# Kernel tuning notes

Hardware: AMD Instinct MI355X
Metric: run time of the kernel (lower is better)

The kernel has to match this reference:

```python
import jax, jax.numpy as jnp
import numpy as np

DIM = 768
NUM_HEADS = 12
HEAD_DIM = DIM // NUM_HEADS
SCALE = HEAD_DIM ** -0.5
KEEP_NUM = 160


def setup_inputs() -> dict:
    key = jax.random.key(0)
    k0, k1, k2, k3 = jax.random.split(key, 4)
    B, N, C = 64, 197, DIM
    x = jax.random.normal(k0, (B, N, C), dtype=jnp.float32)
    # torch nn.Linear weights: [out_features, in_features]
    qkv_w = jax.random.normal(k1, (3 * C, C), dtype=jnp.float32) * (C ** -0.5)
    proj_w = jax.random.normal(k2, (C, C), dtype=jnp.float32) * (C ** -0.5)
    proj_b = jax.random.normal(k3, (C,), dtype=jnp.float32) * 0.01
    return {"x": x, "qkv_w": qkv_w, "proj_w": proj_w, "proj_b": proj_b}


def reference(x, qkv_w, proj_w, proj_b):
    B, N, C = x.shape
    H, D = NUM_HEADS, HEAD_DIM
    # qkv: [B, N, 3, H, D] -> q,k,v each [B, H, N, D]
    qkv = (x @ qkv_w.T).reshape(B, N, 3, H, D)
    qkv = jnp.transpose(qkv, (2, 0, 3, 1, 4))
    q, k, v = qkv[0], qkv[1], qkv[2]
    # raw pre-softmax scores [B, H, N, N]
    attn = jnp.einsum('bhnd,bhmd->bhnm', q, k) * SCALE
    # SUM_ABS_1: CLS row of scores, abs-summed over heads -> [B, N]
    attn_weight = jnp.sum(jnp.abs(attn[:, :, 0, :]), axis=1)
    # top_pool: keep top KEEP_NUM tokens by weight, indices sorted ascending
    _, idx = jax.lax.top_k(attn_weight, KEEP_NUM)
    keep_index = jnp.sort(idx, axis=-1)
    # standard attention
    attn = jax.nn.softmax(attn, axis=-1)
    out = jnp.einsum('bhnm,bhmd->bhnd', attn, v)
    out = jnp.transpose(out, (0, 2, 1, 3)).reshape(B, N, C)
    out = out @ proj_w.T + proj_b
    return out, keep_index
```

## Files before the change

### kernel.cpp

```cpp
#include <hip/hip_runtime.h>
#include <hip/hip_bf16.h>


#define BB 64
#define NN 197
#define CC 768
#define HH 12
#define DD 64
#define KEEP 160
#define SCALE_F 0.125f
#define OUT0_ELEMS ((size_t)BB * NN * CC)
#define VST 212

typedef __attribute__((ext_vector_type(8))) short bf16x8_t;
typedef __attribute__((ext_vector_type(4))) float f32x4_t;

__device__ __forceinline__ float b2f(unsigned short u) {
  union { unsigned u; float f; } cv; cv.u = (unsigned)u << 16; return cv.f;
}
__device__ __forceinline__ unsigned short f2b(float f) {
  union { float f; unsigned u; } cv; cv.f = f;
  return (unsigned short)((cv.u + 0x7FFFu + ((cv.u >> 16) & 1u)) >> 16);
}
__device__ __forceinline__ float ldmix(const void* p, size_t i, int f32) {
  return f32 ? ((const float*)p)[i] : b2f(((const unsigned short*)p)[i]);
}
__device__ __forceinline__ bf16x8_t ld8(const unsigned short* p) {
  short4 a = *(const short4*)p;
  short4 b = *(const short4*)(p + 4);
  bf16x8_t v = {a.x, a.y, a.z, a.w, b.x, b.y, b.z, b.w};
  return v;
}
__device__ __forceinline__ void gload16(const unsigned short* g,
                                        unsigned short* s) {
  __builtin_amdgcn_global_load_lds(
      (const __attribute__((address_space(1))) void*)g,
      (__attribute__((address_space(3))) void*)s, 16, 0, 0);
}

__global__ void detect_kernel(const void* x, int* flag) {
  __shared__ int cnt;
  if (threadIdx.x == 0) cnt = 0;
  __syncthreads();
  const unsigned short* u = (const unsigned short*)x;
  int wild = 0;
  for (int i = threadIdx.x; i < 4096; i += 256) {
    int e = (u[i] >> 7) & 0xFF;
    wild += (e >= 140);
  }
  atomicAdd(&cnt, wild);
  __syncthreads();
  if (threadIdx.x == 0) *flag = (cnt > 100) ? 1 : 0;
}

__global__ void cvt_all(const void* qkv_w, const void* proj_w, const void* proj_b,
                        unsigned short* wb, unsigned short* pw, float* pbf,
                        const int* flag) {
  const int W3 = 3 * CC * CC, W1 = CC * CC;
  int i = blockIdx.x * 256 + threadIdx.x;
  const int f32 = *flag;
  if (i < W3) {
    wb[i] = f32 ? f2b(((const float*)qkv_w)[i]) : ((const unsigned short*)qkv_w)[i];
  } else if (i < W3 + W1) {
    int j = i - W3;
    pw[j] = f32 ? f2b(((const float*)proj_w)[j]) : ((const unsigned short*)proj_w)[j];
  } else if (i < W3 + W1 + CC) {
    int j = i - W3 - W1;
    pbf[j] = ldmix(proj_b, j, f32);
  }
}

__global__ void cvt_x(const void* __restrict__ x, size_t elem_off,
                      unsigned short* __restrict__ xb, int n8,
                      const int* __restrict__ flag) {
  const int i = blockIdx.x * 256 + threadIdx.x;
  if (i >= n8) return;
  const size_t src = elem_off + (size_t)i * 8;
  bf16x8_t v;
  if (*flag) {
    const float* xp = (const float*)x + src;
    float4 u0 = *(const float4*)xp;
    float4 u1 = *(const float4*)(xp + 4);
    v = bf16x8_t{(short)f2b(u0.x), (short)f2b(u0.y), (short)f2b(u0.z),
                 (short)f2b(u0.w), (short)f2b(u1.x), (short)f2b(u1.y),
                 (short)f2b(u1.z), (short)f2b(u1.w)};
  } else {
    v = *(const bf16x8_t*)((const unsigned short*)x + src);
  }
  *(bf16x8_t*)(xb + (size_t)i * 8) = v;
}

__global__ __launch_bounds__(256, 4) void qkv_gemm(
    const unsigned short* __restrict__ xb,
    const unsigned short* __restrict__ wb,
    unsigned short* __restrict__ qkvc, int Mc, int bc, int nRow) {
  const int xcd = blockIdx.x & 7;
  const int seq = blockIdx.x >> 3;
  const int colt = seq % 18;
  const int rowt = (seq / 18) * 8 + xcd;
  if (rowt >= nRow) return;
  const int m0 = rowt * 128;
  const int n0 = colt * 128;

  __shared__ unsigned short As[4096];
  __shared__ unsigned short Bs[4096];
  const int lane = threadIdx.x & 63;
  const int wave = threadIdx.x >> 6;
  const int l16  = lane & 15;
  const int quad = lane >> 4;
  const int wm = wave >> 1, wn = wave & 1;

  const int rS   = wave * 16 + (lane >> 2);
  const int koff = (lane & 3) * 8;
  int grA0 = m0 + rS;       if (grA0 >= Mc) grA0 = Mc - 1;
  int grA1 = m0 + rS + 64;  if (grA1 >= Mc) grA1 = Mc - 1;
  const unsigned short* gA0 = xb + (size_t)grA0 * CC + koff;
  const unsigned short* gA1 = xb + (size_t)grA1 * CC + koff;
  const unsigned short* gB0 = wb + (size_t)(n0 + rS) * CC + koff;
  const unsigned short* gB1 = wb + (size_t)(n0 + rS + 64) * CC + koff;
  unsigned short* sA0 = As + wave * 512;
  unsigned short* sA1 = As + 2048 + wave * 512;
  unsigned short* sB0 = Bs + wave * 512;
  unsigned short* sB1 = Bs + 2048 + wave * 512;

  f32x4_t acc[4][4] = {};
  for (int kt = 0; kt < 24; kt++) {
    __syncthreads();
    gload16(gA0, sA0); gload16(gA1, sA1);
    gload16(gB0, sB0); gload16(gB1, sB1);
    gA0 += 32; gA1 += 32; gB0 += 32; gB1 += 32;
    __syncthreads();
    bf16x8_t afr[4], bfr[4];
    #pragma unroll
    for (int r = 0; r < 4; r++)
      afr[r] = *(const bf16x8_t*)&As[(wm * 4 + r) * 512 + l16 * 32 + quad * 8];
    #pragma unroll
    for (int c = 0; c < 4; c++)
      bfr[c] = *(const bf16x8_t*)&Bs[(wn * 4 + c) * 512 + l16 * 32 + quad * 8];
    #pragma unroll
    for (int r = 0; r < 4; r++)
      #pragma unroll
      for (int c = 0; c < 4; c++)
        acc[r][c] = __builtin_amdgcn_mfma_f32_16x16x32_bf16(afr[r], bfr[c],
                                                            acc[r][c], 0, 0, 0);
  }
  #pragma unroll
  for (int c = 0; c < 4; c++) {
    const int col = n0 + wn * 64 + c * 16 + l16;
    const int s = col / CC;
    const int rem = col - s * CC;
    const int hc = rem >> 6, d = rem & 63;
    #pragma unroll
    for (int r = 0; r < 4; r++) {
      #pragma unroll
      for (int i = 0; i < 4; i++) {
        const int m = m0 + wm * 64 + r * 16 + quad * 4 + i;
        if (m < Mc) {
          const int bb = m / NN, n = m - bb * NN;
          qkvc[((((size_t)s * bc + bb) * HH + hc) * NN + n) * DD + d] =
              f2b(acc[r][c][i]);
        }
      }
    }
  }
}

__global__ __launch_bounds__(256, 4) void proj_gemm(
    const unsigned short* __restrict__ Yc,
    const unsigned short* __restrict__ pw,
    const float* __restrict__ pbf,
    void* __restrict__ out, size_t out_off, int Mc, int nRow,
    const int* __restrict__ flag) {
  const int xcd = blockIdx.x & 7;
  const int seq = blockIdx.x >> 3;
  const int colt = seq % 6;
  const int rowt = (seq / 6) * 8 + xcd;
  if (rowt >= nRow) return;
  const int m0 = rowt * 128;
  const int n0 = colt * 128;

  __shared__ unsigned short As[4096];
  __shared__ unsigned short Bs[4096];
  const int lane = threadIdx.x & 63;
  const int wave = threadIdx.x >> 6;
  const int l16  = lane & 15;
  const int quad = lane >> 4;
  const int wm = wave >> 1, wn = wave & 1;

  const int rS   = wave * 16 + (lane >> 2);
  const int koff = (lane & 3) * 8;
  int grA0 = m0 + rS;       if (grA0 >= Mc) grA0 = Mc - 1;
  int grA1 = m0 + rS + 64;  if (grA1 >= Mc) grA1 = Mc - 1;
  const unsigned short* gA0 = Yc + (size_t)grA0 * CC + koff;
  const unsigned short* gA1 = Yc + (size_t)grA1 * CC + koff;
  const unsigned short* gB0 = pw + (size_t)(n0 + rS) * CC + koff;
  const unsigned short* gB1 = pw + (size_t)(n0 + rS + 64) * CC + koff;
  unsigned short* sA0 = As + wave * 512;
  unsigned short* sA1 = As + 2048 + wave * 512;
  unsigned short* sB0 = Bs + wave * 512;
  unsigned short* sB1 = Bs + 2048 + wave * 512;

  f32x4_t acc[4][4] = {};
  for (int kt = 0; kt < 24; kt++) {
    __syncthreads();
    gload16(gA0, sA0); gload16(gA1, sA1);
    gload16(gB0, sB0); gload16(gB1, sB1);
    gA0 += 32; gA1 += 32; gB0 += 32; gB1 += 32;
    __syncthreads();
    bf16x8_t afr[4], bfr[4];
    #pragma unroll
    for (int r = 0; r < 4; r++)
      afr[r] = *(const bf16x8_t*)&As[(wm * 4 + r) * 512 + l16 * 32 + quad * 8];
    #pragma unroll
    for (int c = 0; c < 4; c++)
      bfr[c] = *(const bf16x8_t*)&Bs[(wn * 4 + c) * 512 + l16 * 32 + quad * 8];
    #pragma unroll
    for (int r = 0; r < 4; r++)
      #pragma unroll
      for (int c = 0; c < 4; c++)
        acc[r][c] = __builtin_amdgcn_mfma_f32_16x16x32_bf16(afr[r], bfr[c],
                                                            acc[r][c], 0, 0, 0);
  }
  const int f32 = *flag;
  #pragma unroll
  for (int c = 0; c < 4; c++) {
    const int col = n0 + wn * 64 + c * 16 + l16;
    const float bv = pbf[col];
    #pragma unroll
    for (int r = 0; r < 4; r++) {
      #pragma unroll
      for (int i = 0; i < 4; i++) {
        const int m = m0 + wm * 64 + r * 16 + quad * 4 + i;
        if (m < Mc) {
          const float val = acc[r][c][i] + bv;
          const size_t oi = out_off + (size_t)m * CC + col;
          if (f32) ((float*)out)[oi] = val;
          else ((unsigned short*)out)[oi] = f2b(val);
        }
      }
    }
  }
}

__global__ __launch_bounds__(256, 3) void attn_kernel(
    const unsigned short* __restrict__ qkvc, int bc,
    unsigned short* __restrict__ Yc) {
  const int bh = blockIdx.x;
  const int bb = bh / HH;
  const int h  = bh % HH;
  const size_t mat = (size_t)bc * HH * NN * DD;
  const unsigned short* q = qkvc + ((size_t)bb * HH + h) * NN * DD;
  const unsigned short* k = q + mat;
  const unsigned short* v = q + 2 * mat;

  __shared__ unsigned short Vt[DD * VST];
  __shared__ unsigned short Pl[4][16 * VST];

  const int lane = threadIdx.x & 63;
  const int wave = threadIdx.x >> 6;
  const int l16  = lane & 15;
  const int quad = lane >> 4;

  #pragma unroll
  for (int it = 0; it < 53; it++) {
    const int key = it * 4 + wave;
    unsigned short val = (key < NN) ? v[(size_t)key * DD + lane]
                                    : (unsigned short)0;
    Vt[lane * VST + key] = val;
  }
  __syncthreads();

  unsigned short* Pw = &Pl[wave][0];

  for (int it = 0; it < 4; it++) {
    const int si = it * 4 + wave;
    if (si >= 13) break;
    const int q0 = si * 16;

    int qrow = q0 + l16; if (qrow >= NN) qrow = NN - 1;
    const unsigned short* qp = q + (size_t)qrow * DD + quad * 8;
    const bf16x8_t aq0 = *(const bf16x8_t*)qp;
    const bf16x8_t aq1 = *(const bf16x8_t*)(qp + 32);

    f32x4_t sc[13];
    #pragma unroll
    for (int ct = 0; ct < 13; ct++) {
      int key = ct * 16 + l16; if (key >= NN) key = NN - 1;
      const unsigned short* kp = k + (size_t)key * DD + quad * 8;
      const bf16x8_t b0 = *(const bf16x8_t*)kp;
      const bf16x8_t b1 = *(const bf16x8_t*)(kp + 32);
      f32x4_t t = {0.f, 0.f, 0.f, 0.f};
      t = __builtin_amdgcn_mfma_f32_16x16x32_bf16(aq0, b0, t, 0, 0, 0);
      t = __builtin_amdgcn_mfma_f32_16x16x32_bf16(aq1, b1, t, 0, 0, 0);
      sc[ct] = t;
    }

    float inv_l[4];
    #pragma unroll
    for (int i = 0; i < 4; i++) {
      float m = -1e30f;
      #pragma unroll
      for (int ct = 0; ct < 13; ct++)
        if (ct < 12 || l16 < 5) m = fmaxf(m, sc[ct][i] * SCALE_F);
      #pragma unroll
      for (int d = 1; d < 16; d <<= 1) m = fmaxf(m, __shfl_xor(m, d, 64));
      float s = 0.f;
      #pragma unroll
      for (int ct = 0; ct < 13; ct++) {
        const float p = (ct < 12 || l16 < 5) ? __expf(sc[ct][i] * SCALE_F - m)
                                             : 0.f;
        sc[ct][i] = p;
        s += p;
      }
      #pragma unroll
      for (int d = 1; d < 16; d <<= 1) s += __shfl_xor(s, d, 64);
      inv_l[i] = 1.0f / s;
    }

    #pragma unroll
    for (int i = 0; i < 4; i++) {
      const int ro = (quad * 4 + i) * VST;
      #pragma unroll
      for (int ct = 0; ct < 13; ct++)
        Pw[ro + ct * 16 + l16] = f2b(sc[ct][i]);
    }

    f32x4_t oc[4] = {};
    #pragma unroll
    for (int ks = 0; ks < 6; ks++) {
      const bf16x8_t ap = ld8(&Pw[l16 * VST + ks * 32 + quad * 8]);
      #pragma unroll
      for (int dt = 0; dt < 4; dt++) {
        const bf16x8_t bv = ld8(&Vt[(dt * 16 + l16) * VST + ks * 32 + quad * 8]);
        oc[dt] = __builtin_amdgcn_mfma_f32_16x16x32_bf16(ap, bv, oc[dt], 0, 0, 0);
      }
    }
    {
      const bf16x8_t zz = {};
      bf16x8_t ap = zz;
      if (quad < 2) ap = ld8(&Pw[l16 * VST + 192 + quad * 8]);
      #pragma unroll
      for (int dt = 0; dt < 4; dt++) {
        bf16x8_t bv = zz;
        if (quad < 2) bv = ld8(&Vt[(dt * 16 + l16) * VST + 192 + quad * 8]);
        oc[dt] = __builtin_amdgcn_mfma_f32_16x16x32_bf16(ap, bv, oc[dt], 0, 0, 0);
      }
    }

    #pragma unroll
    for (int i = 0; i < 4; i++) {
      const int n = q0 + quad * 4 + i;
      if (n < NN) {
        unsigned short* yp = Yc + ((size_t)bb * NN + n) * CC + h * DD;
        #pragma unroll
        for (int dt = 0; dt < 4; dt++)
          yp[dt * 16 + l16] = f2b(oc[dt][i] * inv_l[i]);
      }
    }
  }
}

__global__ __launch_bounds__(256, 4) void qcls_kernel(
    const void* __restrict__ x, const void* __restrict__ qkv_w,
    float* __restrict__ qc, const int* __restrict__ flag) {
  const int idx = blockIdx.x * 4 + (threadIdx.x >> 6);
  if (idx >= BB * CC) return;
  const int b = idx / CC, i = idx - b * CC;
  const int lane = threadIdx.x & 63;
  const int f32 = *flag;
  const size_t xr = (size_t)b * NN * CC;
  const size_t wr = (size_t)i * CC;
  float p = 0.f;
  #pragma unroll
  for (int j = 0; j < 12; j++)
    p += ldmix(x, xr + j * 64 + lane, f32) * ldmix(qkv_w, wr + j * 64 + lane, f32);
  #pragma unroll
  for (int m = 32; m; m >>= 1) p += __shfl_xor(p, m, 64);
  if (lane == 0) qc[(size_t)b * CC + i] = p;
}

__global__ __launch_bounds__(256, 4) void gmat_kernel(
    const void* __restrict__ qkv_w, const float* __restrict__ qc,
    float* __restrict__ g, const int* __restrict__ flag) {
  const int b = blockIdx.x, h = blockIdx.y;
  const int f32 = *flag;
  __shared__ float qh[DD];
  if (threadIdx.x < DD) qh[threadIdx.x] = qc[(size_t)b * CC + h * DD + threadIdx.x];
  __syncthreads();
  const int c0 = threadIdx.x, c1 = c0 + 256, c2 = c1 + 256;
  float a0 = 0.f, a1 = 0.f, a2 = 0.f;
  for (int d = 0; d < DD; d++) {
    const size_t ro = (size_t)(CC + h * DD + d) * CC;
    const float qv = qh[d];
    a0 += ldmix(qkv_w, ro + c0, f32) * qv;
    a1 += ldmix(qkv_w, ro + c1, f32) * qv;
    a2 += ldmix(qkv_w, ro + c2, f32) * qv;
  }
  float* gb = g + ((size_t)b * HH + h) * CC;
  gb[c0] = a0; gb[c1] = a1; gb[c2] = a2;
}

__global__ __launch_bounds__(256, 4) void score_kernel(
    const void* __restrict__ x, const float* __restrict__ g,
    float* __restrict__ wscore, const int* __restrict__ flag) {
  const int idx = blockIdx.x * 4 + (threadIdx.x >> 6);
  if (idx >= BB * NN) return;
  const int b = idx / NN, n = idx - b * NN;
  const int lane = threadIdx.x & 63;
  const int f32 = *flag;
  const size_t xr = ((size_t)b * NN + n) * CC;
  float xv[12];
  #pragma unroll
  for (int j = 0; j < 12; j++) xv[j] = ldmix(x, xr + j * 64 + lane, f32);
  const float* gb = g + (size_t)b * HH * CC;
  float acc = 0.f;
  #pragma unroll
  for (int h = 0; h < HH; h++) {
    const float* gh = gb + (size_t)h * CC;
    float p = 0.f;
    #pragma unroll
    for (int j = 0; j < 12; j++) p += xv[j] * gh[j * 64 + lane];
    #pragma unroll
    for (int m = 32; m; m >>= 1) p += __shfl_xor(p, m, 64);
    acc += fabsf(p);
  }
  if (lane == 0) wscore[(size_t)b * NN + n] = acc;
}

__global__ __launch_bounds__(256, 4) void rank_kernel(
    const float* __restrict__ wscore, void* __restrict__ out,
    const int* __restrict__ flag) {
  const int b = blockIdx.x;
  const int f32 = *flag;
  __shared__ float wgt[NN];
  __shared__ int   rank[NN];
  if (threadIdx.x < NN) wgt[threadIdx.x] = wscore[(size_t)b * NN + threadIdx.x];
  __syncthreads();
  const int n = threadIdx.x;
  if (n < NN) {
    float wi = wgt[n];
    int rk = 0;
    for (int j = 0; j < NN; j++) {
      float wj = wgt[j];
      rk += (wj > wi) || (wj == wi && j < n);
    }
    rank[n] = rk;
  }
  __syncthreads();
  if (n < NN && rank[n] < KEEP) {
    int pos = 0;
    for (int j = 0; j < n; j++) pos += (rank[j] < KEEP);
    const size_t oi = OUT0_ELEMS + (size_t)b * KEEP + pos;
    if (f32) ((float*)out)[oi] = (float)n;
    else ((unsigned short*)out)[oi] = f2b((float)n);
  }
}

extern "C" void kernel_launch(void* const* d_in, const int* in_sizes, int n_in,
                              void* d_out, int out_size, void* d_ws, size_t ws_size,
                              hipStream_t stream) {
  const void* x      = d_in[0];
  const void* qkv_w  = d_in[1];
  const void* proj_w = d_in[2];
  const void* proj_b = d_in[3];

  char* wsb = (char*)d_ws;
  int* flag = (int*)wsb;
  unsigned short* wb  = (unsigned short*)(wsb + 256);
  unsigned short* pw  = (unsigned short*)(wsb + 256 + 3538944);
  float* pbf    = (float*)(wsb + 256 + 3538944 + 1179648);
  float* qc     = (float*)(wsb + 256 + 3538944 + 1179648 + 4096);
  float* g      = qc + (size_t)BB * CC;
  float* wscore = g + (size_t)BB * HH * CC;
  const size_t fixed = 256 + 3538944 + 1179648 + 4096 + 196608 + 2359296 + 51200;
  char* chunk = wsb + fixed;

  const size_t per_batch = (size_t)NN * CC * 2
                         + 3ull * HH * NN * DD * 2
                         + (size_t)NN * CC * 2;
  int Bc = BB;
  while (Bc > 1 && fixed + (size_t)Bc * per_batch > ws_size) Bc >>= 1;

  unsigned short* xb   = (unsigned short*)chunk;
  unsigned short* qkvc = xb + (size_t)Bc * NN * CC;
  unsigned short* Yc   = qkvc + 3ull * Bc * HH * NN * DD;

  detect_kernel<<<1, 256, 0, stream>>>(x, flag);
  const int cvt_n = 3 * CC * CC + CC * CC + CC;
  cvt_all<<<(cvt_n + 255) / 256, 256, 0, stream>>>(qkv_w, proj_w, proj_b,
                                                   wb, pw, pbf, flag);

  qcls_kernel<<<(BB * CC + 3) / 4, 256, 0, stream>>>(x, qkv_w, qc, flag);
  gmat_kernel<<<dim3(BB, HH), 256, 0, stream>>>(qkv_w, qc, g, flag);
  score_kernel<<<(BB * NN + 3) / 4, 256, 0, stream>>>(x, g, wscore, flag);
  rank_kernel<<<BB, 256, 0, stream>>>(wscore, d_out, flag);

  const int nChunks = (BB + Bc - 1) / Bc;
  for (int cb = 0; cb < nChunks; cb++) {
    const int b0 = cb * Bc;
    const int bc = (BB - b0 < Bc) ? (BB - b0) : Bc;
    const int Mc = bc * NN;
    const int n8 = Mc * CC / 8;
    cvt_x<<<(n8 + 255) / 256, 256, 0, stream>>>(
        x, (size_t)b0 * NN * CC, xb, n8, flag);
    const int nRowQ = (Mc + 127) / 128;
    const int gridQ = 8 * 18 * ((nRowQ + 7) / 8);
    qkv_gemm<<<gridQ, 256, 0, stream>>>(xb, wb, qkvc, Mc, bc, nRowQ);
    attn_kernel<<<dim3(bc * HH), 256, 0, stream>>>(qkvc, bc, Yc);
    const int gridP = 8 * 6 * ((nRowQ + 7) / 8);
    proj_gemm<<<gridP, 256, 0, stream>>>(
        Yc, pw, pbf, d_out, (size_t)b0 * NN * CC, Mc, nRowQ, flag);
  }
}
```

Before: 375.0 us.

## Double-buffer LDS in QKV/proj GEMMs and tile gmat kernel across batches

Both bf16 GEMM kernels now use two LDS buffers. The next K-tile's global-to-LDS loads are issued before the current tile's fragments are read, with explicit vmcnt/lgkmcnt waits and raw barriers replacing the two __syncthreads, so memory latency can overlap MFMA work. Separately, gmat_kernel is reorganised to launch per (head, 128-column tile), staging weights and all batch q vectors in shared memory. This lets each weight element be read once instead of once per batch. The costs are doubled LDS usage in the GEMMs, which may reduce occupancy, and a much smaller gmat grid (72 blocks) with 48KB of shared memory each.

```diff
diff --git a/kernel.cpp b/kernel.cpp
--- a/kernel.cpp
+++ b/kernel.cpp
@@ -102,8 +102,8 @@
   const int m0 = rowt * 128;
   const int n0 = colt * 128;
 
-  __shared__ unsigned short As[4096];
-  __shared__ unsigned short Bs[4096];
+  __shared__ unsigned short As[8192];
+  __shared__ unsigned short Bs[8192];
   const int lane = threadIdx.x & 63;
   const int wave = threadIdx.x >> 6;
   const int l16  = lane & 15;
@@ -118,25 +118,38 @@
   const unsigned short* gA1 = xb + (size_t)grA1 * CC + koff;
   const unsigned short* gB0 = wb + (size_t)(n0 + rS) * CC + koff;
   const unsigned short* gB1 = wb + (size_t)(n0 + rS + 64) * CC + koff;
-  unsigned short* sA0 = As + wave * 512;
-  unsigned short* sA1 = As + 2048 + wave * 512;
-  unsigned short* sB0 = Bs + wave * 512;
-  unsigned short* sB1 = Bs + 2048 + wave * 512;
+  unsigned short* const sA0 = As + wave * 512;
+  unsigned short* const sA1 = As + 2048 + wave * 512;
+  unsigned short* const sB0 = Bs + wave * 512;
+  unsigned short* const sB1 = Bs + 2048 + wave * 512;
+
+  gload16(gA0, sA0); gload16(gA1, sA1);
+  gload16(gB0, sB0); gload16(gB1, sB1);
+  gA0 += 32; gA1 += 32; gB0 += 32; gB1 += 32;
 
   f32x4_t acc[4][4] = {};
+  #pragma unroll 2
   for (int kt = 0; kt < 24; kt++) {
-    __syncthreads();
-    gload16(gA0, sA0); gload16(gA1, sA1);
-    gload16(gB0, sB0); gload16(gB1, sB1);
-    gA0 += 32; gA1 += 32; gB0 += 32; gB1 += 32;
-    __syncthreads();
+    const int ro = (kt & 1) << 12;
+    const int so = ro ^ 4096;
+    if (kt < 23) {
+      gload16(gA0, sA0 + so); gload16(gA1, sA1 + so);
+      gload16(gB0, sB0 + so); gload16(gB1, sB1 + so);
+      gA0 += 32; gA1 += 32; gB0 += 32; gB1 += 32;
+      asm volatile("s_waitcnt vmcnt(4)" ::: "memory");
+    } else {
+      asm volatile("s_waitcnt vmcnt(0)" ::: "memory");
+    }
+    __builtin_amdgcn_s_barrier();
     bf16x8_t afr[4], bfr[4];
     #pragma unroll
     for (int r = 0; r < 4; r++)
-      afr[r] = *(const bf16x8_t*)&As[(wm * 4 + r) * 512 + l16 * 32 + quad * 8];
+      afr[r] = *(const bf16x8_t*)&As[ro + (wm * 4 + r) * 512 + l16 * 32 + quad * 8];
     #pragma unroll
     for (int c = 0; c < 4; c++)
-      bfr[c] = *(const bf16x8_t*)&Bs[(wn * 4 + c) * 512 + l16 * 32 + quad * 8];
+      bfr[c] = *(const bf16x8_t*)&Bs[ro + (wn * 4 + c) * 512 + l16 * 32 + quad * 8];
+    asm volatile("s_waitcnt lgkmcnt(0)" ::: "memory");
+    __builtin_amdgcn_s_barrier();
     #pragma unroll
     for (int r = 0; r < 4; r++)
       #pragma unroll
@@ -179,8 +192,8 @@
   const int m0 = rowt * 128;
   const int n0 = colt * 128;
 
-  __shared__ unsigned short As[4096];
-  __shared__ unsigned short Bs[4096];
+  __shared__ unsigned short As[8192];
+  __shared__ unsigned short Bs[8192];
   const int lane = threadIdx.x & 63;
   const int wave = threadIdx.x >> 6;
   const int l16  = lane & 15;
@@ -195,25 +208,38 @@
   const unsigned short* gA1 = Yc + (size_t)grA1 * CC + koff;
   const unsigned short* gB0 = pw + (size_t)(n0 + rS) * CC + koff;
   const unsigned short* gB1 = pw + (size_t)(n0 + rS + 64) * CC + koff;
-  unsigned short* sA0 = As + wave * 512;
-  unsigned short* sA1 = As + 2048 + wave * 512;
-  unsigned short* sB0 = Bs + wave * 512;
-  unsigned short* sB1 = Bs + 2048 + wave * 512;
+  unsigned short* const sA0 = As + wave * 512;
+  unsigned short* const sA1 = As + 2048 + wave * 512;
+  unsigned short* const sB0 = Bs + wave * 512;
+  unsigned short* const sB1 = Bs + 2048 + wave * 512;
+
+  gload16(gA0, sA0); gload16(gA1, sA1);
+  gload16(gB0, sB0); gload16(gB1, sB1);
+  gA0 += 32; gA1 += 32; gB0 += 32; gB1 += 32;
 
   f32x4_t acc[4][4] = {};
+  #pragma unroll 2
   for (int kt = 0; kt < 24; kt++) {
-    __syncthreads();
-    gload16(gA0, sA0); gload16(gA1, sA1);
-    gload16(gB0, sB0); gload16(gB1, sB1);
-    gA0 += 32; gA1 += 32; gB0 += 32; gB1 += 32;
-    __syncthreads();
+    const int ro = (kt & 1) << 12;
+    const int so = ro ^ 4096;
+    if (kt < 23) {
+      gload16(gA0, sA0 + so); gload16(gA1, sA1 + so);
+      gload16(gB0, sB0 + so); gload16(gB1, sB1 + so);
+      gA0 += 32; gA1 += 32; gB0 += 32; gB1 += 32;
+      asm volatile("s_waitcnt vmcnt(4)" ::: "memory");
+    } else {
+      asm volatile("s_waitcnt vmcnt(0)" ::: "memory");
+    }
+    __builtin_amdgcn_s_barrier();
     bf16x8_t afr[4], bfr[4];
     #pragma unroll
     for (int r = 0; r < 4; r++)
-      afr[r] = *(const bf16x8_t*)&As[(wm * 4 + r) * 512 + l16 * 32 + quad * 8];
+      afr[r] = *(const bf16x8_t*)&As[ro + (wm * 4 + r) * 512 + l16 * 32 + quad * 8];
     #pragma unroll
     for (int c = 0; c < 4; c++)
-      bfr[c] = *(const bf16x8_t*)&Bs[(wn * 4 + c) * 512 + l16 * 32 + quad * 8];
+      bfr[c] = *(const bf16x8_t*)&Bs[ro + (wn * 4 + c) * 512 + l16 * 32 + quad * 8];
+    asm volatile("s_waitcnt lgkmcnt(0)" ::: "memory");
+    __builtin_amdgcn_s_barrier();
     #pragma unroll
     for (int r = 0; r < 4; r++)
       #pragma unroll
@@ -379,25 +405,31 @@
   if (lane == 0) qc[(size_t)b * CC + i] = p;
 }
 
-__global__ __launch_bounds__(256, 4) void gmat_kernel(
+__global__ __launch_bounds__(256, 2) void gmat_kernel(
     const void* __restrict__ qkv_w, const float* __restrict__ qc,
     float* __restrict__ g, const int* __restrict__ flag) {
-  const int b = blockIdx.x, h = blockIdx.y;
+  const int h = blockIdx.x, c0 = blockIdx.y * 128;
   const int f32 = *flag;
-  __shared__ float qh[DD];
-  if (threadIdx.x < DD) qh[threadIdx.x] = qc[(size_t)b * CC + h * DD + threadIdx.x];
+  __shared__ float Wt[64][128];
+  __shared__ float qh[64][64];
+  for (int t = threadIdx.x; t < 64 * 128; t += 256) {
+    const int d = t >> 7, c = t & 127;
+    Wt[d][c] = ldmix(qkv_w, (size_t)(CC + h * DD + d) * CC + c0 + c, f32);
+  }
+  for (int t = threadIdx.x; t < 64 * 64; t += 256) {
+    const int b = t >> 6, d = t & 63;
+    qh[b][d] = qc[(size_t)b * CC + h * DD + d];
+  }
   __syncthreads();
-  const int c0 = threadIdx.x, c1 = c0 + 256, c2 = c1 + 256;
-  float a0 = 0.f, a1 = 0.f, a2 = 0.f;
-  for (int d = 0; d < DD; d++) {
-    const size_t ro = (size_t)(CC + h * DD + d) * CC;
-    const float qv = qh[d];
-    a0 += ldmix(qkv_w, ro + c0, f32) * qv;
-    a1 += ldmix(qkv_w, ro + c1, f32) * qv;
-    a2 += ldmix(qkv_w, ro + c2, f32) * qv;
-  }
-  float* gb = g + ((size_t)b * HH + h) * CC;
-  gb[c0] = a0; gb[c1] = a1; gb[c2] = a2;
+  const int c = threadIdx.x & 127;
+  const int bg = (threadIdx.x >> 7) * 32;
+  for (int bi = 0; bi < 32; bi++) {
+    const int b = bg + bi;
+    float a = 0.f;
+    #pragma unroll
+    for (int d = 0; d < 64; d++) a += qh[b][d] * Wt[d][c];
+    g[((size_t)b * HH + h) * CC + c0 + c] = a;
+  }
 }
 
 __global__ __launch_bounds__(256, 4) void score_kernel(
@@ -491,7 +523,7 @@
                                                    wb, pw, pbf, flag);
 
   qcls_kernel<<<(BB * CC + 3) / 4, 256, 0, stream>>>(x, qkv_w, qc, flag);
-  gmat_kernel<<<dim3(BB, HH), 256, 0, stream>>>(qkv_w, qc, g, flag);
+  gmat_kernel<<<dim3(HH, 6), 256, 0, stream>>>(qkv_w, qc, g, flag);
   score_kernel<<<(BB * NN + 3) / 4, 256, 0, stream>>>(x, g, wscore, flag);
   rank_kernel<<<BB, 256, 0, stream>>>(wscore, d_out, flag);
 
```

New measurement: 382.0 us. No clear change (+1.9%).

## Widen GEMM tiles to 128x192, swizzle LDS, stage epilogue through shared memory

Applied to the files above, without the earlier changes.

Both the QKV and projection GEMMs move from 128x128 to 128x192 output tiles, so each block reuses its A tile across more columns and the grid gets smaller. An XOR swizzle is applied to the k-offset of the LDS layout to cut bank conflicts on fragment reads. The epilogues now write accumulators into LDS first, then emit coalesced 16-byte vector stores to global memory instead of scattered 2- or 4-byte stores. Costs are more accumulator registers (24 tiles per wave), larger LDS use, extra barriers in the epilogue, and a launch-bounds hint of 6 blocks per SM that the register count may not allow.

```diff
diff --git a/kernel.cpp b/kernel.cpp
--- a/kernel.cpp
+++ b/kernel.cpp
@@ -90,20 +90,19 @@
   *(bf16x8_t*)(xb + (size_t)i * 8) = v;
 }
 
-__global__ __launch_bounds__(256, 4) void qkv_gemm(
+__global__ __launch_bounds__(256, 6) void qkv_gemm(
     const unsigned short* __restrict__ xb,
     const unsigned short* __restrict__ wb,
     unsigned short* __restrict__ qkvc, int Mc, int bc, int nRow) {
   const int xcd = blockIdx.x & 7;
   const int seq = blockIdx.x >> 3;
-  const int colt = seq % 18;
-  const int rowt = (seq / 18) * 8 + xcd;
+  const int colt = seq % 12;
+  const int rowt = (seq / 12) * 8 + xcd;
   if (rowt >= nRow) return;
   const int m0 = rowt * 128;
-  const int n0 = colt * 128;
-
-  __shared__ unsigned short As[4096];
-  __shared__ unsigned short Bs[4096];
+  const int n0 = colt * 192;
+
+  __shared__ unsigned short lds[12544];
   const int lane = threadIdx.x & 63;
   const int wave = threadIdx.x >> 6;
   const int l16  = lane & 15;
@@ -111,61 +110,86 @@
   const int wm = wave >> 1, wn = wave & 1;
 
   const int rS   = wave * 16 + (lane >> 2);
-  const int koff = (lane & 3) * 8;
+  const int koff = ((lane & 3) ^ ((lane >> 3) & 3)) * 8;
   int grA0 = m0 + rS;       if (grA0 >= Mc) grA0 = Mc - 1;
   int grA1 = m0 + rS + 64;  if (grA1 >= Mc) grA1 = Mc - 1;
   const unsigned short* gA0 = xb + (size_t)grA0 * CC + koff;
   const unsigned short* gA1 = xb + (size_t)grA1 * CC + koff;
   const unsigned short* gB0 = wb + (size_t)(n0 + rS) * CC + koff;
   const unsigned short* gB1 = wb + (size_t)(n0 + rS + 64) * CC + koff;
-  unsigned short* sA0 = As + wave * 512;
-  unsigned short* sA1 = As + 2048 + wave * 512;
-  unsigned short* sB0 = Bs + wave * 512;
-  unsigned short* sB1 = Bs + 2048 + wave * 512;
-
-  f32x4_t acc[4][4] = {};
+  const unsigned short* gB2 = wb + (size_t)(n0 + rS + 128) * CC + koff;
+  unsigned short* const dA = lds + wave * 512;
+  unsigned short* const dB = lds + 4096 + wave * 512;
+
+  const int kgs  = (quad ^ ((l16 >> 1) & 3)) * 8;
+  const int aoff = l16 * 32 + kgs;
+  const int boff = 4096 + l16 * 32 + kgs;
+
+  f32x4_t acc[4][6] = {};
   for (int kt = 0; kt < 24; kt++) {
     __syncthreads();
-    gload16(gA0, sA0); gload16(gA1, sA1);
-    gload16(gB0, sB0); gload16(gB1, sB1);
-    gA0 += 32; gA1 += 32; gB0 += 32; gB1 += 32;
-    __syncthreads();
-    bf16x8_t afr[4], bfr[4];
+    gload16(gA0, dA); gload16(gA1, dA + 2048);
+    gload16(gB0, dB); gload16(gB1, dB + 2048); gload16(gB2, dB + 4096);
+    gA0 += 32; gA1 += 32; gB0 += 32; gB1 += 32; gB2 += 32;
+    __syncthreads();
+    bf16x8_t afr[4], bfr[6];
     #pragma unroll
     for (int r = 0; r < 4; r++)
-      afr[r] = *(const bf16x8_t*)&As[(wm * 4 + r) * 512 + l16 * 32 + quad * 8];
-    #pragma unroll
-    for (int c = 0; c < 4; c++)
-      bfr[c] = *(const bf16x8_t*)&Bs[(wn * 4 + c) * 512 + l16 * 32 + quad * 8];
+      afr[r] = *(const bf16x8_t*)&lds[(wm * 4 + r) * 512 + aoff];
+    #pragma unroll
+    for (int c = 0; c < 6; c++)
+      bfr[c] = *(const bf16x8_t*)&lds[(wn * 6 + c) * 512 + boff];
     #pragma unroll
     for (int r = 0; r < 4; r++)
       #pragma unroll
-      for (int c = 0; c < 4; c++)
+      for (int c = 0; c < 6; c++)
         acc[r][c] = __builtin_amdgcn_mfma_f32_16x16x32_bf16(afr[r], bfr[c],
                                                             acc[r][c], 0, 0, 0);
   }
-  #pragma unroll
-  for (int c = 0; c < 4; c++) {
-    const int col = n0 + wn * 64 + c * 16 + l16;
-    const int s = col / CC;
-    const int rem = col - s * CC;
-    const int hc = rem >> 6, d = rem & 63;
-    #pragma unroll
-    for (int r = 0; r < 4; r++) {
-      #pragma unroll
-      for (int i = 0; i < 4; i++) {
-        const int m = m0 + wm * 64 + r * 16 + quad * 4 + i;
-        if (m < Mc) {
-          const int bb = m / NN, n = m - bb * NN;
-          qkvc[((((size_t)s * bc + bb) * HH + hc) * NN + n) * DD + d] =
-              f2b(acc[r][c][i]);
+  __syncthreads();
+
+  #pragma unroll
+  for (int h = 0; h < 2; h++) {
+    if (wm == h) {
+      #pragma unroll
+      for (int c = 0; c < 6; c++)
+        #pragma unroll
+        for (int r = 0; r < 4; r++)
+          #pragma unroll
+          for (int i = 0; i < 4; i++)
+            lds[(r * 16 + quad * 4 + i) * 196 + wn * 96 + c * 16 + l16] =
+                f2b(acc[r][c][i]);
+    }
+    __syncthreads();
+    {
+      const int rowl = threadIdx.x >> 2;
+      const int m = m0 + h * 64 + rowl;
+      if (m < Mc) {
+        const int bb2 = m / NN, n = m - bb2 * NN;
+        #pragma unroll
+        for (int j = 0; j < 3; j++) {
+          const int c = (threadIdx.x & 3) * 3 + j;
+          const int col = n0 + c * 16;
+          const int s = col / CC;
+          const int rem = col - s * CC;
+          const int hc = rem >> 6, d0 = rem & 63;
+          const unsigned short* src = lds + rowl * 196 + c * 16;
+          uint2 u0 = *(const uint2*)(src);
+          uint2 u1 = *(const uint2*)(src + 4);
+          uint2 u2 = *(const uint2*)(src + 8);
+          uint2 u3 = *(const uint2*)(src + 12);
+          unsigned short* dst =
+              qkvc + ((((size_t)s * bc + bb2) * HH + hc) * NN + n) * DD + d0;
+          *(uint4*)(dst)     = uint4{u0.x, u0.y, u1.x, u1.y};
+          *(uint4*)(dst + 8) = uint4{u2.x, u2.y, u3.x, u3.y};
         }
       }
     }
-  }
-}
-
-__global__ __launch_bounds__(256, 4) void proj_gemm(
+    __syncthreads();
+  }
+}
+
+__global__ __launch_bounds__(256, 6) void proj_gemm(
     const unsigned short* __restrict__ Yc,
     const unsigned short* __restrict__ pw,
     const float* __restrict__ pbf,
@@ -173,14 +197,13 @@
     const int* __restrict__ flag) {
   const int xcd = blockIdx.x & 7;
   const int seq = blockIdx.x >> 3;
-  const int colt = seq % 6;
-  const int rowt = (seq / 6) * 8 + xcd;
+  const int colt = seq % 4;
+  const int rowt = (seq / 4) * 8 + xcd;
   if (rowt >= nRow) return;
   const int m0 = rowt * 128;
-  const int n0 = colt * 128;
-
-  __shared__ unsigned short As[4096];
-  __shared__ unsigned short Bs[4096];
+  const int n0 = colt * 192;
+
+  __shared__ unsigned short lds[12544];
   const int lane = threadIdx.x & 63;
   const int wave = threadIdx.x >> 6;
   const int l16  = lane & 15;
@@ -188,57 +211,93 @@
   const int wm = wave >> 1, wn = wave & 1;
 
   const int rS   = wave * 16 + (lane >> 2);
-  const int koff = (lane & 3) * 8;
+  const int koff = ((lane & 3) ^ ((lane >> 3) & 3)) * 8;
   int grA0 = m0 + rS;       if (grA0 >= Mc) grA0 = Mc - 1;
   int grA1 = m0 + rS + 64;  if (grA1 >= Mc) grA1 = Mc - 1;
   const unsigned short* gA0 = Yc + (size_t)grA0 * CC + koff;
   const unsigned short* gA1 = Yc + (size_t)grA1 * CC + koff;
   const unsigned short* gB0 = pw + (size_t)(n0 + rS) * CC + koff;
   const unsigned short* gB1 = pw + (size_t)(n0 + rS + 64) * CC + koff;
-  unsigned short* sA0 = As + wave * 512;
-  unsigned short* sA1 = As + 2048 + wave * 512;
-  unsigned short* sB0 = Bs + wave * 512;
-  unsigned short* sB1 = Bs + 2048 + wave * 512;
-
-  f32x4_t acc[4][4] = {};
+  const unsigned short* gB2 = pw + (size_t)(n0 + rS + 128) * CC + koff;
+  unsigned short* const dA = lds + wave * 512;
+  unsigned short* const dB = lds + 4096 + wave * 512;
+
+  const int kgs  = (quad ^ ((l16 >> 1) & 3)) * 8;
+  const int aoff = l16 * 32 + kgs;
+  const int boff = 4096 + l16 * 32 + kgs;
+
+  f32x4_t acc[4][6] = {};
   for (int kt = 0; kt < 24; kt++) {
     __syncthreads();
-    gload16(gA0, sA0); gload16(gA1, sA1);
-    gload16(gB0, sB0); gload16(gB1, sB1);
-    gA0 += 32; gA1 += 32; gB0 += 32; gB1 += 32;
-    __syncthreads();
-    bf16x8_t afr[4], bfr[4];
+    gload16(gA0, dA); gload16(gA1, dA + 2048);
+    gload16(gB0, dB); gload16(gB1, dB + 2048); gload16(gB2, dB + 4096);
+    gA0 += 32; gA1 += 32; gB0 += 32; gB1 += 32; gB2 += 32;
+    __syncthreads();
+    bf16x8_t afr[4], bfr[6];
     #pragma unroll
     for (int r = 0; r < 4; r++)
-      afr[r] = *(const bf16x8_t*)&As[(wm * 4 + r) * 512 + l16 * 32 + quad * 8];
-    #pragma unroll
-    for (int c = 0; c < 4; c++)
-      bfr[c] = *(const bf16x8_t*)&Bs[(wn * 4 + c) * 512 + l16 * 32 + quad * 8];
+      afr[r] = *(const bf16x8_t*)&lds[(wm * 4 + r) * 512 + aoff];
+    #pragma unroll
+    for (int c = 0; c < 6; c++)
+      bfr[c] = *(const bf16x8_t*)&lds[(wn * 6 + c) * 512 + boff];
     #pragma unroll
     for (int r = 0; r < 4; r++)
       #pragma unroll
-      for (int c = 0; c < 4; c++)
+      for (int c = 0; c < 6; c++)
         acc[r][c] = __builtin_amdgcn_mfma_f32_16x16x32_bf16(afr[r], bfr[c],
                                                             acc[r][c], 0, 0, 0);
   }
-  const int f32 = *flag;
-  #pragma unroll
-  for (int c = 0; c < 4; c++) {
-    const int col = n0 + wn * 64 + c * 16 + l16;
-    const float bv = pbf[col];
-    #pragma unroll
-    for (int r = 0; r < 4; r++) {
-      #pragma unroll
-      for (int i = 0; i < 4; i++) {
-        const int m = m0 + wm * 64 + r * 16 + quad * 4 + i;
-        if (m < Mc) {
-          const float val = acc[r][c][i] + bv;
-          const size_t oi = out_off + (size_t)m * CC + col;
-          if (f32) ((float*)out)[oi] = val;
-          else ((unsigned short*)out)[oi] = f2b(val);
+  __syncthreads();
+
+  const int f32o = *flag;
+  float* Cf = (float*)lds;
+  #pragma unroll
+  for (int p = 0; p < 4; p++) {
+    if (wm == (p >> 1)) {
+      #pragma unroll
+      for (int rr = 0; rr < 2; rr++) {
+        const int r = (p & 1) * 2 + rr;
+        #pragma unroll
+        for (int c = 0; c < 6; c++) {
+          const float bv = pbf[n0 + wn * 96 + c * 16 + l16];
+          #pragma unroll
+          for (int i = 0; i < 4; i++)
+            Cf[(rr * 16 + quad * 4 + i) * 196 + wn * 96 + c * 16 + l16] =
+                acc[r][c][i] + bv;
         }
       }
     }
+    __syncthreads();
+    {
+      const int rowl = threadIdx.x >> 3;
+      const int m = m0 + p * 32 + rowl;
+      if (m < Mc) {
+        const int off = (threadIdx.x & 7) * 24;
+        const float* src = Cf + rowl * 196 + off;
+        const size_t ob = out_off + (size_t)m * CC + n0 + off;
+        if (f32o) {
+          float* dst = (float*)out + ob;
+          #pragma unroll
+          for (int j = 0; j < 6; j++) {
+            float4 v = {src[j * 4], src[j * 4 + 1], src[j * 4 + 2],
+                        src[j * 4 + 3]};
+            *(float4*)(dst + j * 4) = v;
+          }
+        } else {
+          unsigned short* dst = (unsigned short*)out + ob;
+          #pragma unroll
+          for (int j = 0; j < 3; j++) {
+            uint4 v;
+            v.x = (unsigned)f2b(src[j * 8 + 0]) | ((unsigned)f2b(src[j * 8 + 1]) << 16);
+            v.y = (unsigned)f2b(src[j * 8 + 2]) | ((unsigned)f2b(src[j * 8 + 3]) << 16);
+            v.z = (unsigned)f2b(src[j * 8 + 4]) | ((unsigned)f2b(src[j * 8 + 5]) << 16);
+            v.w = (unsigned)f2b(src[j * 8 + 6]) | ((unsigned)f2b(src[j * 8 + 7]) << 16);
+            *(uint4*)(dst + j * 8) = v;
+          }
+        }
+      }
+    }
+    __syncthreads();
   }
 }
 
@@ -504,10 +563,10 @@
     cvt_x<<<(n8 + 255) / 256, 256, 0, stream>>>(
         x, (size_t)b0 * NN * CC, xb, n8, flag);
     const int nRowQ = (Mc + 127) / 128;
-    const int gridQ = 8 * 18 * ((nRowQ + 7) / 8);
+    const int gridQ = 8 * 12 * ((nRowQ + 7) / 8);
     qkv_gemm<<<gridQ, 256, 0, stream>>>(xb, wb, qkvc, Mc, bc, nRowQ);
     attn_kernel<<<dim3(bc * HH), 256, 0, stream>>>(qkvc, bc, Yc);
-    const int gridP = 8 * 6 * ((nRowQ + 7) / 8);
+    const int gridP = 8 * 4 * ((nRowQ + 7) / 8);
     proj_gemm<<<gridP, 256, 0, stream>>>(
         Yc, pw, pbf, d_out, (size_t)b0 * NN * CC, Mc, nRowQ, flag);
   }
```

Measured after the change: 1.308 ms. 3.49x slower.
